# Kernel tuning notes

Hardware: AMD Instinct MI355X
Metric: run time of the kernel (lower is better)

The kernel has to match this reference:

```python
import jax, jax.numpy as jnp
import numpy as np
from jax.scipy.linalg import expm

BATCH = 65536
N_MUSCLES = 8
DT = 0.0166667
NN_RATIO = 0.3


def setup_inputs() -> dict:
    key = jax.random.key(0)
    ks = jax.random.split(key, 16)
    m = N_MUSCLES
    SS = 0.5 * jax.random.normal(ks[0], (BATCH, 2), dtype=jnp.float32)
    Alphas = jax.random.uniform(ks[1], (BATCH, m), dtype=jnp.float32)
    # per-muscle bilinear-model parameters (positive, physically plausible)
    K0s = 1.0 + jax.random.uniform(ks[2], (m,), dtype=jnp.float32)
    K1s = 1.0 + jax.random.uniform(ks[3], (m,), dtype=jnp.float32)
    L0s = 0.5 + 0.1 * jax.random.uniform(ks[4], (m,), dtype=jnp.float32)
    L1s = 0.1 * jax.random.uniform(ks[5], (m,), dtype=jnp.float32)
    Ms = 0.05 * jax.random.normal(ks[6], (m,), dtype=jnp.float32)  # moment arms
    I = jnp.array([0.05], dtype=jnp.float32)   # inertia
    Bv = jnp.array([0.2], dtype=jnp.float32)   # joint damping (self.B)
    Kv = jnp.array([1.0], dtype=jnp.float32)   # joint stiffness (self.K)
    # compensational_nn weights batched over muscles: 3 -> 32 -> 32 -> 32 -> 1
    def lin(k, fo, fi):
        return (jax.random.normal(k, (m, fo, fi)) / np.sqrt(fi)).astype(jnp.float32)
    W1 = lin(ks[7], 32, 3);  b1 = jnp.zeros((m, 32), jnp.float32)
    W2 = lin(ks[8], 32, 32); b2 = jnp.zeros((m, 32), jnp.float32)
    W3 = lin(ks[9], 32, 32); b3 = jnp.zeros((m, 32), jnp.float32)
    W4 = lin(ks[10], 1, 32); b4 = jnp.zeros((m, 1), jnp.float32)
    return dict(SS=SS, Alphas=Alphas, K0s=K0s, K1s=K1s, L0s=L0s, L1s=L1s, Ms=Ms,
                I=I, Bv=Bv, Kv=Kv, W1=W1, b1=b1, W2=W2, b2=b2, W3=W3, b3=b3, W4=W4, b4=b4)


def _forward(SS, Alphas, K0s, K1s, L0s, L1s, Ms, I, Bv, Kv, W1, b1, W2, b2, W3, b3, W4, b4):
    bsz = SS.shape[0]
    a = jnp.clip(Alphas, 0.0, 1.0)                      # [B, m]
    l = SS[:, 0:1] * Ms                                  # [B, m] muscle lengths (w * moment_arm)
    dl = SS[:, 1:2] * Ms                                 # [B, m] muscle speeds
    # compensational NN (dropout = identity in eval mode), batched over muscles
    x = jnp.stack([l, dl, a], axis=-1)                   # [B, m, 3]
    h = jax.nn.leaky_relu(jnp.einsum('bmi,moi->bmo', x, W1) + b1)
    h = jax.nn.leaky_relu(jnp.einsum('bmi,moi->bmo', h, W2) + b2)
    h = jax.nn.leaky_relu(jnp.einsum('bmi,moi->bmo', h, W3) + b3)
    nn_out = jnp.tanh(jnp.einsum('bmi,moi->bmo', h, W4) + b4)[..., 0] * NN_RATIO  # [B, m]
    # continuous-time state matrix A = [[0, 1], [-(K+Kjoint)/I, -(D+Bjoint)/I]]
    Km = (K0s + K1s * a) * Ms * Ms                       # [B, m]
    Ksum = Km.sum(axis=1)                                # [B]
    A10 = -(Ksum + Kv[0]) / I[0]
    D = 2.0 * jnp.sqrt(Ksum * I[0])                      # critical damping term
    A11 = -(D + Bv[0]) / I[0]
    zeros = jnp.zeros_like(A10)
    ones = jnp.ones_like(A10)
    A = jnp.stack([jnp.stack([zeros, ones], axis=-1),
                   jnp.stack([A10, A11], axis=-1)], axis=1)            # [B, 2, 2]
    # input matrix B: row1 = [sum_i B_F_i * M_i / I, 1/I]
    B_F = (K0s + K1s * a) * (L0s + L1s * a - jnp.abs(l)) + K1s * L1s * a * a * nn_out  # [B, m]
    B10 = (B_F * Ms).sum(axis=1) / I[0]                  # [B]
    Brow1 = jnp.stack([B10, ones / I[0]], axis=-1)       # [B, 2]
    Bm = jnp.stack([jnp.zeros((bsz, 2), A.dtype), Brow1], axis=1)       # [B, 2, 2]
    # discretize with linear input interpolation: expm of the 6x6 block matrix
    M6 = jnp.zeros((bsz, 6, 6), A.dtype)
    M6 = M6.at[:, :2, :2].set(A * DT)
    M6 = M6.at[:, :2, 2:4].set(Bm * DT)
    M6 = M6.at[:, 2:4, 4:6].set(jnp.eye(2, dtype=A.dtype))
    E = jax.vmap(expm)(M6)                               # [B, 6, 6]
    Ad = E[:, :2, :2]
    Bd1 = E[:, :2, 4:6]
    Bd0 = E[:, :2, 2:4] - Bd1
    U = jnp.broadcast_to(jnp.array([[1.0], [0.0]], A.dtype), (bsz, 2, 1))  # U0 == U1
    SSout = Ad @ SS[:, :, None] + Bd0 @ U + Bd1 @ U      # [B, 2, 1]
    return SSout


def reference(SS, Alphas, K0s, K1s, L0s, L1s, Ms, I, Bv, Kv, W1, b1, W2, b2, W3, b3, W4, b4):
    SSout = _forward(SS, Alphas, K0s, K1s, L0s, L1s, Ms, I, Bv, Kv,
                     W1, b1, W2, b2, W3, b3, W4, b4)
    return SSout[:, 0:1], SSout[:, :, 0]
```

## Files before the change

### kernel.cpp

```cpp
#include <hip/hip_runtime.h>
#include <math.h>

#define BATCH 65536
#define DT_C 0.0166667f
#define NN_RATIO_C 0.3f

typedef __bf16 bf16x8 __attribute__((ext_vector_type(8)));
typedef unsigned short us8 __attribute__((ext_vector_type(8)));
typedef unsigned short us4 __attribute__((ext_vector_type(4)));
typedef float f32x4 __attribute__((ext_vector_type(4)));

union FragU { us8 u; bf16x8 b; };

__device__ __forceinline__ unsigned short f2bf(float f) {
    unsigned u = __float_as_uint(f);
    u += 0x7FFFu + ((u >> 16) & 1u);
    return (unsigned short)(u >> 16);
}
__device__ __forceinline__ float lrelu(float x) { return x > 0.0f ? x : 0.01f * x; }

__global__ __launch_bounds__(512) void joint_kernel(
    const float* __restrict__ SS, const float* __restrict__ Alphas,
    const float* __restrict__ K0s, const float* __restrict__ K1s,
    const float* __restrict__ L0s, const float* __restrict__ L1s,
    const float* __restrict__ Ms, const float* __restrict__ Ivec,
    const float* __restrict__ Bv, const float* __restrict__ Kv,
    const float* __restrict__ W1, const float* __restrict__ b1,
    const float* __restrict__ W2, const float* __restrict__ b2,
    const float* __restrict__ W3, const float* __restrict__ b3,
    const float* __restrict__ W4, const float* __restrict__ b4,
    float* __restrict__ out)
{
    __shared__ unsigned short Xbuf[8][16 * 40];
    __shared__ float red_k[8][64];
    __shared__ float red_bf[8][64];

    const int tid  = threadIdx.x;
    const int lane = tid & 63;
    const int w    = tid >> 6;
    const int m    = __builtin_amdgcn_readfirstlane(w);
    const int n16  = lane & 15;
    const int quad = lane >> 4;

    const float ms = Ms[m];
    const float k0 = K0s[m], k1 = K1s[m], l0 = L0s[m], l1 = L1s[m];
    const float b4m = b4[m];

    FragU w1f[2], w2f[2], w3f[2];
    f32x4 bias1[2], bias2[2], bias3[2];
    #pragma unroll
    for (int t = 0; t < 2; ++t) {
        const int o = t * 16 + n16;
        const float* p2 = W2 + m * 1024 + o * 32 + quad * 8;
        const float* p3 = W3 + m * 1024 + o * 32 + quad * 8;
        f32x4 a2 = *(const f32x4*)p2, c2 = *(const f32x4*)(p2 + 4);
        f32x4 a3 = *(const f32x4*)p3, c3 = *(const f32x4*)(p3 + 4);
        #pragma unroll
        for (int j = 0; j < 4; ++j) {
            w2f[t].u[j] = f2bf(a2[j]); w2f[t].u[4 + j] = f2bf(c2[j]);
            w3f[t].u[j] = f2bf(a3[j]); w3f[t].u[4 + j] = f2bf(c3[j]);
        }
        us8 z = {0,0,0,0,0,0,0,0};
        w1f[t].u = z;
        if (quad == 0) {
            const float* p1 = W1 + m * 96 + o * 3;
            w1f[t].u[0] = f2bf(p1[0]);
            w1f[t].u[1] = f2bf(p1[1]);
            w1f[t].u[2] = f2bf(p1[2]);
        }
        bias1[t] = *(const f32x4*)(b1 + m * 32 + t * 16 + quad * 4);
        bias2[t] = *(const f32x4*)(b2 + m * 32 + t * 16 + quad * 4);
        bias3[t] = *(const f32x4*)(b3 + m * 32 + t * 16 + quad * 4);
    }
    const f32x4 w4a = *(const f32x4*)(W4 + m * 32 + quad * 4);
    const f32x4 w4b = *(const f32x4*)(W4 + m * 32 + 16 + quad * 4);

    unsigned short* X = &Xbuf[w][0];

    #pragma unroll 1
    for (int s = 0; s < 4; ++s) {
        const int bb = blockIdx.x * 64 + s * 16 + n16;
        const float s0v = SS[2 * bb];
        const float s1v = SS[2 * bb + 1];
        float av = Alphas[8 * bb + m];
        av = fminf(fmaxf(av, 0.0f), 1.0f);
        const float lv  = s0v * ms;
        const float dlv = s1v * ms;

        FragU xf;
        us8 z = {0,0,0,0,0,0,0,0};
        xf.u = z;
        if (quad == 0) { xf.u[0] = f2bf(lv); xf.u[1] = f2bf(dlv); xf.u[2] = f2bf(av); }

        f32x4 acc0 = bias1[0], acc1 = bias1[1];
        acc0 = __builtin_amdgcn_mfma_f32_16x16x32_bf16(w1f[0].b, xf.b, acc0, 0, 0, 0);
        acc1 = __builtin_amdgcn_mfma_f32_16x16x32_bf16(w1f[1].b, xf.b, acc1, 0, 0, 0);

        us4 st0, st1;
        #pragma unroll
        for (int r = 0; r < 4; ++r) {
            st0[r] = f2bf(lrelu(acc0[r]));
            st1[r] = f2bf(lrelu(acc1[r]));
        }
        *(us4*)&X[n16 * 40 + quad * 4]      = st0;
        *(us4*)&X[n16 * 40 + 16 + quad * 4] = st1;
        __asm__ volatile("s_waitcnt lgkmcnt(0)" ::: "memory");

        FragU hf;
        hf.u = *(const us8*)&X[n16 * 40 + quad * 8];
        acc0 = bias2[0]; acc1 = bias2[1];
        acc0 = __builtin_amdgcn_mfma_f32_16x16x32_bf16(w2f[0].b, hf.b, acc0, 0, 0, 0);
        acc1 = __builtin_amdgcn_mfma_f32_16x16x32_bf16(w2f[1].b, hf.b, acc1, 0, 0, 0);

        #pragma unroll
        for (int r = 0; r < 4; ++r) {
            st0[r] = f2bf(lrelu(acc0[r]));
            st1[r] = f2bf(lrelu(acc1[r]));
        }
        *(us4*)&X[n16 * 40 + quad * 4]      = st0;
        *(us4*)&X[n16 * 40 + 16 + quad * 4] = st1;
        __asm__ volatile("s_waitcnt lgkmcnt(0)" ::: "memory");

        hf.u = *(const us8*)&X[n16 * 40 + quad * 8];
        acc0 = bias3[0]; acc1 = bias3[1];
        acc0 = __builtin_amdgcn_mfma_f32_16x16x32_bf16(w3f[0].b, hf.b, acc0, 0, 0, 0);
        acc1 = __builtin_amdgcn_mfma_f32_16x16x32_bf16(w3f[1].b, hf.b, acc1, 0, 0, 0);

        float dot = 0.0f;
        #pragma unroll
        for (int r = 0; r < 4; ++r) {
            dot += lrelu(acc0[r]) * w4a[r];
            dot += lrelu(acc1[r]) * w4b[r];
        }
        dot += __shfl_xor(dot, 16, 64);
        dot += __shfl_xor(dot, 32, 64);

        if (quad == 0) {
            const float x2 = 2.0f * (dot + b4m);
            const float e2x = __expf(x2);
            const float nn = (1.0f - 2.0f / (e2x + 1.0f)) * NN_RATIO_C;
            const float kk = k0 + k1 * av;
            red_k[w][s * 16 + n16]  = kk * ms * ms;
            red_bf[w][s * 16 + n16] = (kk * (l0 + l1 * av - fabsf(lv)) + k1 * l1 * av * av * nn) * ms;
        }
    }

    __syncthreads();

    if (tid < 64) {
        float Ksum = 0.0f, BFsum = 0.0f;
        #pragma unroll
        for (int mm = 0; mm < 8; ++mm) {
            Ksum  += red_k[mm][tid];
            BFsum += red_bf[mm][tid];
        }

        const int b = blockIdx.x * 64 + tid;
        const float s0 = SS[2 * b];
        const float s1 = SS[2 * b + 1];
        const float I  = Ivec[0];
        const float bv = Bv[0];
        const float kv = Kv[0];
        const float inv_I = 1.0f / I;

        const float A10 = -(Ksum + kv) * inv_I;
        const float D   = 2.0f * sqrtf(Ksum * I);
        const float A11 = -(D + bv) * inv_I;
        const float B10 = BFsum * inv_I;

        const float m01 = DT_C;
        const float m10 = A10 * DT_C, m11 = A11 * DT_C, m12 = B10 * DT_C;

        float p00 = 0.0f, p01 = m01, p02 = 0.0f;
        float p10 = m10,  p11 = m11, p12 = m12;
        float t00 = p00, t01 = p01, t02 = p02;
        float t10 = p10, t11 = p11, t12 = p12;
        #pragma unroll
        for (int k = 2; k <= 16; ++k) {
            float inv = 1.0f / (float)k;
            float q00 = (p01 * m10) * inv;
            float q01 = (p00 * m01 + p01 * m11) * inv;
            float q02 = (p01 * m12) * inv;
            float q10 = (p11 * m10) * inv;
            float q11 = (p10 * m01 + p11 * m11) * inv;
            float q12 = (p11 * m12) * inv;
            p00 = q00; p01 = q01; p02 = q02;
            p10 = q10; p11 = q11; p12 = q12;
            t00 += p00; t01 += p01; t02 += p02;
            t10 += p10; t11 += p11; t12 += p12;
        }
        const float E00 = 1.0f + t00, E01 = t01, c0 = t02;
        const float E10 = t10,        E11 = 1.0f + t11, c1 = t12;

        const float o0 = E00 * s0 + E01 * s1 + c0;
        const float o1 = E10 * s0 + E11 * s1 + c1;

        out[b] = o0;
        out[BATCH + 2 * b]     = o0;
        out[BATCH + 2 * b + 1] = o1;
    }
}

extern "C" void kernel_launch(void* const* d_in, const int* in_sizes, int n_in,
                              void* d_out, int out_size, void* d_ws, size_t ws_size,
                              hipStream_t stream) {
    const float* SS     = (const float*)d_in[0];
    const float* Alphas = (const float*)d_in[1];
    const float* K0s    = (const float*)d_in[2];
    const float* K1s    = (const float*)d_in[3];
    const float* L0s    = (const float*)d_in[4];
    const float* L1s    = (const float*)d_in[5];
    const float* Ms     = (const float*)d_in[6];
    const float* I      = (const float*)d_in[7];
    const float* Bv     = (const float*)d_in[8];
    const float* Kv     = (const float*)d_in[9];
    const float* W1     = (const float*)d_in[10];
    const float* b1     = (const float*)d_in[11];
    const float* W2     = (const float*)d_in[12];
    const float* b2     = (const float*)d_in[13];
    const float* W3     = (const float*)d_in[14];
    const float* b3     = (const float*)d_in[15];
    const float* W4     = (const float*)d_in[16];
    const float* b4     = (const float*)d_in[17];
    float* out = (float*)d_out;

    joint_kernel<<<BATCH / 64, 512, 0, stream>>>(
        SS, Alphas, K0s, K1s, L0s, L1s, Ms, I, Bv, Kv,
        W1, b1, W2, b2, W3, b3, W4, b4, out);
}
```

Measured before the change: 109.3 us.

## Interleave two independent MLP tiles per wave and double batch per block

Each wave now processes two 16-sample tiles at once with separate LDS scratch buffers, interleaving their MFMA chains to hide MFMA and LDS latency. The explicit lgkmcnt waits are dropped. Each block covers 128 samples, halving the grid and amortising the weight load and bf16 conversion per block. The manual bf16 rounding is replaced with a native cast, SS is read with float2 loads, and the epilogue now runs on 128 threads. This costs more registers and LDS, and removing the waits relies on the compiler ordering LDS store→load within a wave.

```diff
diff --git a/kernel.cpp b/kernel.cpp
--- a/kernel.cpp
+++ b/kernel.cpp
@@ -13,9 +13,9 @@
 union FragU { us8 u; bf16x8 b; };
 
 __device__ __forceinline__ unsigned short f2bf(float f) {
-    unsigned u = __float_as_uint(f);
-    u += 0x7FFFu + ((u >> 16) & 1u);
-    return (unsigned short)(u >> 16);
+    union { __bf16 h; unsigned short u; } v;
+    v.h = (__bf16)f;
+    return v.u;
 }
 __device__ __forceinline__ float lrelu(float x) { return x > 0.0f ? x : 0.01f * x; }
 
@@ -31,9 +31,9 @@
     const float* __restrict__ W4, const float* __restrict__ b4,
     float* __restrict__ out)
 {
-    __shared__ unsigned short Xbuf[8][16 * 40];
-    __shared__ float red_k[8][64];
-    __shared__ float red_bf[8][64];
+    __shared__ unsigned short Xbuf[16][640];
+    __shared__ float red_k[8][128];
+    __shared__ float red_bf[8][128];
 
     const int tid  = threadIdx.x;
     const int lane = tid & 63;
@@ -75,79 +75,112 @@
     const f32x4 w4a = *(const f32x4*)(W4 + m * 32 + quad * 4);
     const f32x4 w4b = *(const f32x4*)(W4 + m * 32 + 16 + quad * 4);
 
-    unsigned short* X = &Xbuf[w][0];
+    unsigned short* const X0 = &Xbuf[2 * w][0];
+    unsigned short* const X1 = &Xbuf[2 * w + 1][0];
 
     #pragma unroll 1
-    for (int s = 0; s < 4; ++s) {
-        const int bb = blockIdx.x * 64 + s * 16 + n16;
-        const float s0v = SS[2 * bb];
-        const float s1v = SS[2 * bb + 1];
-        float av = Alphas[8 * bb + m];
-        av = fminf(fmaxf(av, 0.0f), 1.0f);
-        const float lv  = s0v * ms;
-        const float dlv = s1v * ms;
-
-        FragU xf;
-        us8 z = {0,0,0,0,0,0,0,0};
-        xf.u = z;
-        if (quad == 0) { xf.u[0] = f2bf(lv); xf.u[1] = f2bf(dlv); xf.u[2] = f2bf(av); }
-
-        f32x4 acc0 = bias1[0], acc1 = bias1[1];
-        acc0 = __builtin_amdgcn_mfma_f32_16x16x32_bf16(w1f[0].b, xf.b, acc0, 0, 0, 0);
-        acc1 = __builtin_amdgcn_mfma_f32_16x16x32_bf16(w1f[1].b, xf.b, acc1, 0, 0, 0);
-
-        us4 st0, st1;
-        #pragma unroll
-        for (int r = 0; r < 4; ++r) {
-            st0[r] = f2bf(lrelu(acc0[r]));
-            st1[r] = f2bf(lrelu(acc1[r]));
-        }
-        *(us4*)&X[n16 * 40 + quad * 4]      = st0;
-        *(us4*)&X[n16 * 40 + 16 + quad * 4] = st1;
-        __asm__ volatile("s_waitcnt lgkmcnt(0)" ::: "memory");
-
-        FragU hf;
-        hf.u = *(const us8*)&X[n16 * 40 + quad * 8];
-        acc0 = bias2[0]; acc1 = bias2[1];
-        acc0 = __builtin_amdgcn_mfma_f32_16x16x32_bf16(w2f[0].b, hf.b, acc0, 0, 0, 0);
-        acc1 = __builtin_amdgcn_mfma_f32_16x16x32_bf16(w2f[1].b, hf.b, acc1, 0, 0, 0);
-
-        #pragma unroll
-        for (int r = 0; r < 4; ++r) {
-            st0[r] = f2bf(lrelu(acc0[r]));
-            st1[r] = f2bf(lrelu(acc1[r]));
-        }
-        *(us4*)&X[n16 * 40 + quad * 4]      = st0;
-        *(us4*)&X[n16 * 40 + 16 + quad * 4] = st1;
-        __asm__ volatile("s_waitcnt lgkmcnt(0)" ::: "memory");
-
-        hf.u = *(const us8*)&X[n16 * 40 + quad * 8];
-        acc0 = bias3[0]; acc1 = bias3[1];
-        acc0 = __builtin_amdgcn_mfma_f32_16x16x32_bf16(w3f[0].b, hf.b, acc0, 0, 0, 0);
-        acc1 = __builtin_amdgcn_mfma_f32_16x16x32_bf16(w3f[1].b, hf.b, acc1, 0, 0, 0);
-
-        float dot = 0.0f;
-        #pragma unroll
-        for (int r = 0; r < 4; ++r) {
-            dot += lrelu(acc0[r]) * w4a[r];
-            dot += lrelu(acc1[r]) * w4b[r];
-        }
-        dot += __shfl_xor(dot, 16, 64);
-        dot += __shfl_xor(dot, 32, 64);
+    for (int s = 0; s < 8; s += 2) {
+        float lv[2], dlv[2], av[2];
+        FragU xf[2];
+        #pragma unroll
+        for (int p = 0; p < 2; ++p) {
+            const int bb = blockIdx.x * 128 + (s + p) * 16 + n16;
+            const float2 ssv = *(const float2*)&SS[2 * bb];
+            float a = Alphas[8 * bb + m];
+            a = fminf(fmaxf(a, 0.0f), 1.0f);
+            av[p]  = a;
+            lv[p]  = ssv.x * ms;
+            dlv[p] = ssv.y * ms;
+            us8 z = {0,0,0,0,0,0,0,0};
+            xf[p].u = z;
+            if (quad == 0) {
+                xf[p].u[0] = f2bf(lv[p]);
+                xf[p].u[1] = f2bf(dlv[p]);
+                xf[p].u[2] = f2bf(a);
+            }
+        }
+
+        f32x4 acc0[2], acc1[2];
+        #pragma unroll
+        for (int p = 0; p < 2; ++p) {
+            acc0[p] = __builtin_amdgcn_mfma_f32_16x16x32_bf16(w1f[0].b, xf[p].b, bias1[0], 0, 0, 0);
+            acc1[p] = __builtin_amdgcn_mfma_f32_16x16x32_bf16(w1f[1].b, xf[p].b, bias1[1], 0, 0, 0);
+        }
+        #pragma unroll
+        for (int p = 0; p < 2; ++p) {
+            unsigned short* X = p ? X1 : X0;
+            us4 st0, st1;
+            #pragma unroll
+            for (int r = 0; r < 4; ++r) {
+                st0[r] = f2bf(lrelu(acc0[p][r]));
+                st1[r] = f2bf(lrelu(acc1[p][r]));
+            }
+            *(us4*)&X[n16 * 40 + quad * 4]      = st0;
+            *(us4*)&X[n16 * 40 + 16 + quad * 4] = st1;
+        }
+
+        FragU hf[2];
+        #pragma unroll
+        for (int p = 0; p < 2; ++p)
+            hf[p].u = *(const us8*)&((p ? X1 : X0)[n16 * 40 + quad * 8]);
+        #pragma unroll
+        for (int p = 0; p < 2; ++p) {
+            acc0[p] = __builtin_amdgcn_mfma_f32_16x16x32_bf16(w2f[0].b, hf[p].b, bias2[0], 0, 0, 0);
+            acc1[p] = __builtin_amdgcn_mfma_f32_16x16x32_bf16(w2f[1].b, hf[p].b, bias2[1], 0, 0, 0);
+        }
+        #pragma unroll
+        for (int p = 0; p < 2; ++p) {
+            unsigned short* X = p ? X1 : X0;
+            us4 st0, st1;
+            #pragma unroll
+            for (int r = 0; r < 4; ++r) {
+                st0[r] = f2bf(lrelu(acc0[p][r]));
+                st1[r] = f2bf(lrelu(acc1[p][r]));
+            }
+            *(us4*)&X[n16 * 40 + quad * 4]      = st0;
+            *(us4*)&X[n16 * 40 + 16 + quad * 4] = st1;
+        }
+
+        #pragma unroll
+        for (int p = 0; p < 2; ++p)
+            hf[p].u = *(const us8*)&((p ? X1 : X0)[n16 * 40 + quad * 8]);
+        #pragma unroll
+        for (int p = 0; p < 2; ++p) {
+            acc0[p] = __builtin_amdgcn_mfma_f32_16x16x32_bf16(w3f[0].b, hf[p].b, bias3[0], 0, 0, 0);
+            acc1[p] = __builtin_amdgcn_mfma_f32_16x16x32_bf16(w3f[1].b, hf[p].b, bias3[1], 0, 0, 0);
+        }
+
+        float dot[2];
+        #pragma unroll
+        for (int p = 0; p < 2; ++p) {
+            float d = 0.0f;
+            #pragma unroll
+            for (int r = 0; r < 4; ++r) {
+                d += lrelu(acc0[p][r]) * w4a[r];
+                d += lrelu(acc1[p][r]) * w4b[r];
+            }
+            d += __shfl_xor(d, 16, 64);
+            d += __shfl_xor(d, 32, 64);
+            dot[p] = d;
+        }
 
         if (quad == 0) {
-            const float x2 = 2.0f * (dot + b4m);
-            const float e2x = __expf(x2);
-            const float nn = (1.0f - 2.0f / (e2x + 1.0f)) * NN_RATIO_C;
-            const float kk = k0 + k1 * av;
-            red_k[w][s * 16 + n16]  = kk * ms * ms;
-            red_bf[w][s * 16 + n16] = (kk * (l0 + l1 * av - fabsf(lv)) + k1 * l1 * av * av * nn) * ms;
+            #pragma unroll
+            for (int p = 0; p < 2; ++p) {
+                const float x2 = 2.0f * (dot[p] + b4m);
+                const float e2x = __expf(x2);
+                const float nn = (1.0f - 2.0f / (e2x + 1.0f)) * NN_RATIO_C;
+                const float kk = k0 + k1 * av[p];
+                red_k[w][(s + p) * 16 + n16]  = kk * ms * ms;
+                red_bf[w][(s + p) * 16 + n16] =
+                    (kk * (l0 + l1 * av[p] - fabsf(lv[p])) + k1 * l1 * av[p] * av[p] * nn) * ms;
+            }
         }
     }
 
     __syncthreads();
 
-    if (tid < 64) {
+    if (tid < 128) {
         float Ksum = 0.0f, BFsum = 0.0f;
         #pragma unroll
         for (int mm = 0; mm < 8; ++mm) {
@@ -155,9 +188,9 @@
             BFsum += red_bf[mm][tid];
         }
 
-        const int b = blockIdx.x * 64 + tid;
-        const float s0 = SS[2 * b];
-        const float s1 = SS[2 * b + 1];
+        const int b = blockIdx.x * 128 + tid;
+        const float2 ssv = *(const float2*)&SS[2 * b];
+        const float s0 = ssv.x, s1 = ssv.y;
         const float I  = Ivec[0];
         const float bv = Bv[0];
         const float kv = Kv[0];
@@ -224,7 +257,7 @@
     const float* b4     = (const float*)d_in[17];
     float* out = (float*)d_out;
 
-    joint_kernel<<<BATCH / 64, 512, 0, stream>>>(
+    joint_kernel<<<BATCH / 128, 512, 0, stream>>>(
         SS, Alphas, K0s, K1s, L0s, L1s, Ms, I, Bv, Kv,
         W1, b1, W2, b2, W3, b3, W4, b4, out);
 }
```

Measured after the change: 103.8 us. 5.0% less time.
